# Optimization experiments

Measured on AMD Instinct MI355X. Metric: run time of the kernel, lower is better.

## Reference

```python
import jax, jax.numpy as jnp
import numpy as np
from jax import lax

WIN = 7            # skimage default win_size
K1, K2 = 0.01, 0.03
DATA_RANGE = 1.0


def _uniform_filter_valid(x):
    # (skimage uses reflect-padded uniform_filter then crops pad=3, which equals
    #  a valid windowed mean.)
    c, h, w = x.shape
    x4 = x[:, None]                                   # (C,1,H,W)
    kh = jnp.full((1, 1, WIN, 1), 1.0 / WIN, x.dtype)
    kw = jnp.full((1, 1, 1, WIN), 1.0 / WIN, x.dtype)
    dn = ('NCHW', 'OIHW', 'NCHW')
    x4 = lax.conv_general_dilated(x4, kh, (1, 1), 'VALID', dimension_numbers=dn)
    x4 = lax.conv_general_dilated(x4, kw, (1, 1), 'VALID', dimension_numbers=dn)
    return x4[:, 0]


def setup_inputs() -> dict:
    key = jax.random.key(0)
    k1, k2 = jax.random.split(key)
    shape = (32, 3, 512, 512)
    return {
        'input_tensor': jax.random.uniform(k1, shape, dtype=jnp.float32),
        'target': jax.random.uniform(k2, shape, dtype=jnp.float32),
    }


def reference(input_tensor, target):
    h, w = input_tensor.shape[-2:]
    x = input_tensor.reshape(-1, h, w).astype(jnp.float32)
    y = target.reshape(-1, h, w).astype(jnp.float32)

    C1 = (K1 * DATA_RANGE) ** 2
    C2 = (K2 * DATA_RANGE) ** 2
    NP = WIN * WIN
    cov_norm = NP / (NP - 1.0)  # sample covariance (skimage default)

    ux = _uniform_filter_valid(x)
    uy = _uniform_filter_valid(y)
    uxx = _uniform_filter_valid(x * x)
    uyy = _uniform_filter_valid(y * y)
    uxy = _uniform_filter_valid(x * y)

    vx = cov_norm * (uxx - ux * ux)
    vy = cov_norm * (uyy - uy * uy)
    vxy = cov_norm * (uxy - ux * uy)

    S = ((2.0 * ux * uy + C1) * (2.0 * vxy + C2)) / (
        (ux * ux + uy * uy + C1) * (vx + vy + C2))
    # mean over cropped spatial map per channel, then over channels == global mean
    return jnp.mean(S)
```

## Files before the change

### kernel.cpp

```cpp
#include <hip/hip_runtime.h>


namespace {
constexpr int W      = 512;
constexpr int HH     = 512;
constexpr int NIMG   = 96;
constexpr int OW     = 506;
constexpr int RSTRIP = 23;
constexpr int NSTRIP = 22;
constexpr float D1      = 0.2401f;
constexpr float D2      = 2.1609f;
constexpr float COVN    = 49.0f / 48.0f;
constexpr float COV2    = 2.0f * COVN;
constexpr float K49COV  = 49.0f * COVN;
constexpr float K49COV2 = 2.0f * 49.0f * COVN;
constexpr double NPIX   = 96.0 * 506.0 * 506.0;
}

__global__ __launch_bounds__(64, 3) void ssim_main(const float* __restrict__ X,
                                                   const float* __restrict__ Y,
                                                   double* __restrict__ acc)
{
    const int lane = threadIdx.x;
    const int img  = blockIdx.y;
    const int r0   = blockIdx.x * RSTRIP;
    const int c0   = lane * 8;

    const float* xb = X + (size_t)img * (W * HH) + c0;
    const float* yb = Y + (size_t)img * (W * HH) + c0;

    float V[5][8];
#pragma unroll
    for (int q = 0; q < 5; q++)
#pragma unroll
        for (int i = 0; i < 8; i++) V[q][i] = 0.0f;

    float xr[8], yr[8], xo[8], yo[8];

    auto load_row = [&](int r, float (&dx)[8], float (&dy)[8]) {
        const float* px = xb + (size_t)r * W;
        const float* py = yb + (size_t)r * W;
        float4 a = *(const float4*)px;
        float4 b = *(const float4*)(px + 4);
        dx[0] = a.x; dx[1] = a.y; dx[2] = a.z; dx[3] = a.w;
        dx[4] = b.x; dx[5] = b.y; dx[6] = b.z; dx[7] = b.w;
        float4 e = *(const float4*)py;
        float4 f = *(const float4*)(py + 4);
        dy[0] = e.x; dy[1] = e.y; dy[2] = e.z; dy[3] = e.w;
        dy[4] = f.x; dy[5] = f.y; dy[6] = f.z; dy[7] = f.w;
    };

#pragma unroll
    for (int k = 0; k < 6; k++) {
        load_row(r0 + k, xr, yr);
#pragma unroll
        for (int i = 0; i < 8; i++) {
            V[0][i] += xr[i];
            V[1][i] += yr[i];
            V[2][i] = fmaf(xr[i], xr[i], V[2][i]);
            V[3][i] = fmaf(yr[i], yr[i], V[3][i]);
            V[4][i] = fmaf(xr[i], yr[i], V[4][i]);
        }
    }
    load_row(r0 + 6, xr, yr);

    float sacc = 0.0f;

    for (int j = 0; j < RSTRIP; j++) {
#pragma unroll
        for (int i = 0; i < 8; i++) {
            V[0][i] += xr[i];
            V[1][i] += yr[i];
            V[2][i] = fmaf(xr[i], xr[i], V[2][i]);
            V[3][i] = fmaf(yr[i], yr[i], V[3][i]);
            V[4][i] = fmaf(xr[i], yr[i], V[4][i]);
        }

        load_row(r0 + j, xo, yo);
        int rn = r0 + j + 7; if (rn > HH - 1) rn = HH - 1;
        load_row(rn, xr, yr);

        float Vh[5][6];
#pragma unroll
        for (int q = 0; q < 5; q++)
#pragma unroll
            for (int i = 0; i < 6; i++) Vh[q][i] = __shfl_down(V[q][i], 1);

        float H[5];
#pragma unroll
        for (int q = 0; q < 5; q++)
            H[q] = ((V[q][0] + V[q][1]) + (V[q][2] + V[q][3])) +
                   ((V[q][4] + V[q][5]) + V[q][6]);

#pragma unroll
        for (int i = 0; i < 8; i++) {
            float U0 = H[0], U1 = H[1], U2 = H[2], U3 = H[3], U4 = H[4];
            float A    = U0 * U1;
            float q01  = fmaf(U0, U0, U1 * U1);
            float num1 = fmaf(2.0f, A, D1);
            float den1 = q01 + D1;
            float num2 = fmaf(K49COV2, U4, fmaf(-COV2, A, D2));
            float s23  = U2 + U3;
            float den2 = fmaf(K49COV, s23, fmaf(-COVN, q01, D2));
            float S = (num1 * num2) * __builtin_amdgcn_rcpf(den1 * den2);
            sacc += (c0 + i < OW) ? S : 0.0f;
            if (i < 7) {
#pragma unroll
                for (int q = 0; q < 5; q++) {
                    float addv = (i == 0) ? V[q][7] : Vh[q][i - 1];
                    H[q] += addv - V[q][i];
                }
            }
        }

#pragma unroll
        for (int i = 0; i < 8; i++) {
            V[0][i] -= xo[i];
            V[1][i] -= yo[i];
            V[2][i] = fmaf(-xo[i], xo[i], V[2][i]);
            V[3][i] = fmaf(-yo[i], yo[i], V[3][i]);
            V[4][i] = fmaf(-xo[i], yo[i], V[4][i]);
        }
    }

#pragma unroll
    for (int off = 32; off > 0; off >>= 1)
        sacc += __shfl_down(sacc, off);
    if (lane == 0) atomicAdd(acc, (double)sacc);
}

__global__ void ssim_finalize(const double* __restrict__ acc, float* __restrict__ out)
{
    out[0] = (float)(acc[0] / NPIX);
}

extern "C" void kernel_launch(void* const* d_in, const int* in_sizes, int n_in,
                              void* d_out, int out_size, void* d_ws, size_t ws_size,
                              hipStream_t stream)
{
    const float* X = (const float*)d_in[0];
    const float* Y = (const float*)d_in[1];
    float* out = (float*)d_out;
    double* acc = (double*)d_ws;

    hipMemsetAsync(d_ws, 0, sizeof(double), stream);
    ssim_main<<<dim3(NSTRIP, NIMG), 64, 0, stream>>>(X, Y, acc);
    ssim_finalize<<<1, 1, 0, stream>>>(acc, out);
}
```

Measured before the change: 253.1 us.

## Process two output rows per iteration with two-row-ahead prefetch and full unroll

Restructures the sliding-window loop to handle two output rows per iteration, loading two old and two new rows at a time so more memory loads are in flight ahead of use. The strip is re-split to 22 rows across 23 strips so the row count is even, and the loop is fully unrolled. Occupancy hint is relaxed from 3 to 2 waves per SIMD to allow more registers for the larger prefetch buffers. This trades occupancy and code size for deeper per-thread memory-level parallelism.

```diff
diff --git a/kernel.cpp b/kernel.cpp
--- a/kernel.cpp
+++ b/kernel.cpp
@@ -6,8 +6,8 @@
 constexpr int HH     = 512;
 constexpr int NIMG   = 96;
 constexpr int OW     = 506;
-constexpr int RSTRIP = 23;
-constexpr int NSTRIP = 22;
+constexpr int RSTRIP = 22;
+constexpr int NSTRIP = 23;
 constexpr float D1      = 0.2401f;
 constexpr float D2      = 2.1609f;
 constexpr float COVN    = 49.0f / 48.0f;
@@ -17,7 +17,7 @@
 constexpr double NPIX   = 96.0 * 506.0 * 506.0;
 }
 
-__global__ __launch_bounds__(64, 3) void ssim_main(const float* __restrict__ X,
+__global__ __launch_bounds__(64, 2) void ssim_main(const float* __restrict__ X,
                                                    const float* __restrict__ Y,
                                                    double* __restrict__ acc)
 {
@@ -35,63 +35,61 @@
 #pragma unroll
         for (int i = 0; i < 8; i++) V[q][i] = 0.0f;
 
-    float xr[8], yr[8], xo[8], yo[8];
-
-    auto load_row = [&](int r, float (&dx)[8], float (&dy)[8]) {
-        const float* px = xb + (size_t)r * W;
-        const float* py = yb + (size_t)r * W;
-        float4 a = *(const float4*)px;
-        float4 b = *(const float4*)(px + 4);
-        dx[0] = a.x; dx[1] = a.y; dx[2] = a.z; dx[3] = a.w;
-        dx[4] = b.x; dx[5] = b.y; dx[6] = b.z; dx[7] = b.w;
-        float4 e = *(const float4*)py;
-        float4 f = *(const float4*)(py + 4);
-        dy[0] = e.x; dy[1] = e.y; dy[2] = e.z; dy[3] = e.w;
-        dy[4] = f.x; dy[5] = f.y; dy[6] = f.z; dy[7] = f.w;
+    auto load2 = [&](int r, float (&dx)[2][8], float (&dy)[2][8]) {
+        int ra = r;     if (ra > HH - 1) ra = HH - 1;
+        int rb = r + 1; if (rb > HH - 1) rb = HH - 1;
+        const float* pxa = xb + (size_t)ra * W;
+        const float* pxb = xb + (size_t)rb * W;
+        const float* pya = yb + (size_t)ra * W;
+        const float* pyb = yb + (size_t)rb * W;
+        float4 a0 = *(const float4*)pxa, a1 = *(const float4*)(pxa + 4);
+        float4 b0 = *(const float4*)pxb, b1 = *(const float4*)(pxb + 4);
+        float4 e0 = *(const float4*)pya, e1 = *(const float4*)(pya + 4);
+        float4 f0 = *(const float4*)pyb, f1 = *(const float4*)(pyb + 4);
+        dx[0][0]=a0.x; dx[0][1]=a0.y; dx[0][2]=a0.z; dx[0][3]=a0.w;
+        dx[0][4]=a1.x; dx[0][5]=a1.y; dx[0][6]=a1.z; dx[0][7]=a1.w;
+        dx[1][0]=b0.x; dx[1][1]=b0.y; dx[1][2]=b0.z; dx[1][3]=b0.w;
+        dx[1][4]=b1.x; dx[1][5]=b1.y; dx[1][6]=b1.z; dx[1][7]=b1.w;
+        dy[0][0]=e0.x; dy[0][1]=e0.y; dy[0][2]=e0.z; dy[0][3]=e0.w;
+        dy[0][4]=e1.x; dy[0][5]=e1.y; dy[0][6]=e1.z; dy[0][7]=e1.w;
+        dy[1][0]=f0.x; dy[1][1]=f0.y; dy[1][2]=f0.z; dy[1][3]=f0.w;
+        dy[1][4]=f1.x; dy[1][5]=f1.y; dy[1][6]=f1.z; dy[1][7]=f1.w;
     };
 
-#pragma unroll
-    for (int k = 0; k < 6; k++) {
-        load_row(r0 + k, xr, yr);
+    auto vadd = [&](const float (&xs)[8], const float (&ys)[8]) {
 #pragma unroll
         for (int i = 0; i < 8; i++) {
-            V[0][i] += xr[i];
-            V[1][i] += yr[i];
-            V[2][i] = fmaf(xr[i], xr[i], V[2][i]);
-            V[3][i] = fmaf(yr[i], yr[i], V[3][i]);
-            V[4][i] = fmaf(xr[i], yr[i], V[4][i]);
+            V[0][i] += xs[i];
+            V[1][i] += ys[i];
+            V[2][i] = fmaf(xs[i], xs[i], V[2][i]);
+            V[3][i] = fmaf(ys[i], ys[i], V[3][i]);
+            V[4][i] = fmaf(xs[i], ys[i], V[4][i]);
         }
-    }
-    load_row(r0 + 6, xr, yr);
+    };
+    auto vsub = [&](const float (&xs)[8], const float (&ys)[8]) {
+#pragma unroll
+        for (int i = 0; i < 8; i++) {
+            V[0][i] -= xs[i];
+            V[1][i] -= ys[i];
+            V[2][i] = fmaf(-xs[i], xs[i], V[2][i]);
+            V[3][i] = fmaf(-ys[i], ys[i], V[3][i]);
+            V[4][i] = fmaf(-xs[i], ys[i], V[4][i]);
+        }
+    };
 
     float sacc = 0.0f;
 
-    for (int j = 0; j < RSTRIP; j++) {
-#pragma unroll
-        for (int i = 0; i < 8; i++) {
-            V[0][i] += xr[i];
-            V[1][i] += yr[i];
-            V[2][i] = fmaf(xr[i], xr[i], V[2][i]);
-            V[3][i] = fmaf(yr[i], yr[i], V[3][i]);
-            V[4][i] = fmaf(xr[i], yr[i], V[4][i]);
-        }
-
-        load_row(r0 + j, xo, yo);
-        int rn = r0 + j + 7; if (rn > HH - 1) rn = HH - 1;
-        load_row(rn, xr, yr);
-
+    auto ssim_row = [&]() {
         float Vh[5][6];
 #pragma unroll
         for (int q = 0; q < 5; q++)
 #pragma unroll
             for (int i = 0; i < 6; i++) Vh[q][i] = __shfl_down(V[q][i], 1);
-
         float H[5];
 #pragma unroll
         for (int q = 0; q < 5; q++)
             H[q] = ((V[q][0] + V[q][1]) + (V[q][2] + V[q][3])) +
                    ((V[q][4] + V[q][5]) + V[q][6]);
-
 #pragma unroll
         for (int i = 0; i < 8; i++) {
             float U0 = H[0], U1 = H[1], U2 = H[2], U3 = H[3], U4 = H[4];
@@ -112,14 +110,40 @@
                 }
             }
         }
+    };
+
+    {
+        float tx[2][8], ty[2][8];
+#pragma unroll
+        for (int k = 0; k < 3; k++) {
+            load2(r0 + 2 * k, tx, ty);
+            vadd(tx[0], ty[0]);
+            vadd(tx[1], ty[1]);
+        }
+    }
+
+    float xc[2][8], yc[2][8];
+    load2(r0 + 6, xc, yc);
+
+#pragma unroll
+    for (int jj = 0; jj < RSTRIP / 2; jj++) {
+        const int j0 = r0 + 2 * jj;
+
+        float xo[2][8], yo[2][8], xn[2][8], yn[2][8];
+        load2(j0, xo, yo);
+        load2(j0 + 8, xn, yn);
+
+        vadd(xc[0], yc[0]);
+        ssim_row();
+        vadd(xc[1], yc[1]);
+        vsub(xo[0], yo[0]);
+        ssim_row();
+        vsub(xo[1], yo[1]);
 
 #pragma unroll
         for (int i = 0; i < 8; i++) {
-            V[0][i] -= xo[i];
-            V[1][i] -= yo[i];
-            V[2][i] = fmaf(-xo[i], xo[i], V[2][i]);
-            V[3][i] = fmaf(-yo[i], yo[i], V[3][i]);
-            V[4][i] = fmaf(-xo[i], yo[i], V[4][i]);
+            xc[0][i] = xn[0][i]; xc[1][i] = xn[1][i];
+            yc[0][i] = yn[0][i]; yc[1][i] = yn[1][i];
         }
     }
 
```

Measured after the change: 251.8 us. About the same (-0.5%).

## Cache sliding-window rows in LDS ring buffer and lengthen row strips

Applied to the files above, without the earlier changes.

Rows that leave the vertical 7-row window are now read back from a per-block shared-memory ring buffer instead of being fetched again from global memory, which roughly halves global loads per output row. Strips are doubled to 46 rows, halving the grid and the redundant 6-row warmup per strip, and accumulation is spread over per-image atomics to reduce contention on one address. In exchange the grid has fewer blocks (11x96) and each block uses 32KB of LDS, which may limit occupancy and latency hiding.

```diff
diff --git a/kernel.cpp b/kernel.cpp
--- a/kernel.cpp
+++ b/kernel.cpp
@@ -6,8 +6,8 @@
 constexpr int HH     = 512;
 constexpr int NIMG   = 96;
 constexpr int OW     = 506;
-constexpr int RSTRIP = 23;
-constexpr int NSTRIP = 22;
+constexpr int RSTRIP = 46;
+constexpr int NSTRIP = 11;
 constexpr float D1      = 0.2401f;
 constexpr float D2      = 2.1609f;
 constexpr float COVN    = 49.0f / 48.0f;
@@ -17,10 +17,12 @@
 constexpr double NPIX   = 96.0 * 506.0 * 506.0;
 }
 
-__global__ __launch_bounds__(64, 3) void ssim_main(const float* __restrict__ X,
-                                                   const float* __restrict__ Y,
-                                                   double* __restrict__ acc)
+__global__ __launch_bounds__(64) void ssim_main(const float* __restrict__ X,
+                                                const float* __restrict__ Y,
+                                                double* __restrict__ acc)
 {
+    __shared__ float ring[8 * 1024];
+
     const int lane = threadIdx.x;
     const int img  = blockIdx.y;
     const int r0   = blockIdx.x * RSTRIP;
@@ -29,15 +31,18 @@
     const float* xb = X + (size_t)img * (W * HH) + c0;
     const float* yb = Y + (size_t)img * (W * HH) + c0;
 
+    float* ringx = &ring[c0];
+    float* ringy = &ring[512 + c0];
+
     float V[5][8];
 #pragma unroll
     for (int q = 0; q < 5; q++)
 #pragma unroll
         for (int i = 0; i < 8; i++) V[q][i] = 0.0f;
 
-    float xr[8], yr[8], xo[8], yo[8];
+    float xr[8], yr[8];
 
-    auto load_row = [&](int r, float (&dx)[8], float (&dy)[8]) {
+    auto gload_row = [&](int r, float (&dx)[8], float (&dy)[8]) {
         const float* px = xb + (size_t)r * W;
         const float* py = yb + (size_t)r * W;
         float4 a = *(const float4*)px;
@@ -49,36 +54,58 @@
         dy[0] = e.x; dy[1] = e.y; dy[2] = e.z; dy[3] = e.w;
         dy[4] = f.x; dy[5] = f.y; dy[6] = f.z; dy[7] = f.w;
     };
+    auto ring_write = [&](int slot, const float (&dx)[8], const float (&dy)[8]) {
+        float* px = ringx + slot * 1024;
+        float* py = ringy + slot * 1024;
+        *(float4*)(px)     = make_float4(dx[0], dx[1], dx[2], dx[3]);
+        *(float4*)(px + 4) = make_float4(dx[4], dx[5], dx[6], dx[7]);
+        *(float4*)(py)     = make_float4(dy[0], dy[1], dy[2], dy[3]);
+        *(float4*)(py + 4) = make_float4(dy[4], dy[5], dy[6], dy[7]);
+    };
+    auto ring_read = [&](int slot, float (&dx)[8], float (&dy)[8]) {
+        const float* px = ringx + slot * 1024;
+        const float* py = ringy + slot * 1024;
+        float4 a = *(const float4*)px;
+        float4 b = *(const float4*)(px + 4);
+        dx[0] = a.x; dx[1] = a.y; dx[2] = a.z; dx[3] = a.w;
+        dx[4] = b.x; dx[5] = b.y; dx[6] = b.z; dx[7] = b.w;
+        float4 e = *(const float4*)py;
+        float4 f = *(const float4*)(py + 4);
+        dy[0] = e.x; dy[1] = e.y; dy[2] = e.z; dy[3] = e.w;
+        dy[4] = f.x; dy[5] = f.y; dy[6] = f.z; dy[7] = f.w;
+    };
+    auto vadd = [&](const float (&xs)[8], const float (&ys)[8]) {
+#pragma unroll
+        for (int i = 0; i < 8; i++) {
+            V[0][i] += xs[i];
+            V[1][i] += ys[i];
+            V[2][i] = fmaf(xs[i], xs[i], V[2][i]);
+            V[3][i] = fmaf(ys[i], ys[i], V[3][i]);
+            V[4][i] = fmaf(xs[i], ys[i], V[4][i]);
+        }
+    };
 
 #pragma unroll
     for (int k = 0; k < 6; k++) {
-        load_row(r0 + k, xr, yr);
-#pragma unroll
-        for (int i = 0; i < 8; i++) {
-            V[0][i] += xr[i];
-            V[1][i] += yr[i];
-            V[2][i] = fmaf(xr[i], xr[i], V[2][i]);
-            V[3][i] = fmaf(yr[i], yr[i], V[3][i]);
-            V[4][i] = fmaf(xr[i], yr[i], V[4][i]);
-        }
+        gload_row(r0 + k, xr, yr);
+        vadd(xr, yr);
+        ring_write(k, xr, yr);
     }
-    load_row(r0 + 6, xr, yr);
+    gload_row(r0 + 6, xr, yr);
 
     float sacc = 0.0f;
 
+#pragma unroll 2
     for (int j = 0; j < RSTRIP; j++) {
-#pragma unroll
-        for (int i = 0; i < 8; i++) {
-            V[0][i] += xr[i];
-            V[1][i] += yr[i];
-            V[2][i] = fmaf(xr[i], xr[i], V[2][i]);
-            V[3][i] = fmaf(yr[i], yr[i], V[3][i]);
-            V[4][i] = fmaf(xr[i], yr[i], V[4][i]);
-        }
+        vadd(xr, yr);
+        ring_write((j + 6) & 7, xr, yr);
 
-        load_row(r0 + j, xo, yo);
         int rn = r0 + j + 7; if (rn > HH - 1) rn = HH - 1;
-        load_row(rn, xr, yr);
+        float xn[8], yn[8];
+        gload_row(rn, xn, yn);
+
+        float xo[8], yo[8];
+        ring_read(j & 7, xo, yo);
 
         float Vh[5][6];
 #pragma unroll
@@ -121,17 +148,22 @@
             V[3][i] = fmaf(-yo[i], yo[i], V[3][i]);
             V[4][i] = fmaf(-xo[i], yo[i], V[4][i]);
         }
+
+#pragma unroll
+        for (int i = 0; i < 8; i++) { xr[i] = xn[i]; yr[i] = yn[i]; }
     }
 
 #pragma unroll
     for (int off = 32; off > 0; off >>= 1)
         sacc += __shfl_down(sacc, off);
-    if (lane == 0) atomicAdd(acc, (double)sacc);
+    if (lane == 0) atomicAdd(&acc[img], (double)sacc);
 }
 
 __global__ void ssim_finalize(const double* __restrict__ acc, float* __restrict__ out)
 {
-    out[0] = (float)(acc[0] / NPIX);
+    double s = 0.0;
+    for (int i = 0; i < NIMG; i++) s += acc[i];
+    out[0] = (float)(s / NPIX);
 }
 
 extern "C" void kernel_launch(void* const* d_in, const int* in_sizes, int n_in,
@@ -143,7 +175,7 @@
     float* out = (float*)d_out;
     double* acc = (double*)d_ws;
 
-    hipMemsetAsync(d_ws, 0, sizeof(double), stream);
+    hipMemsetAsync(d_ws, 0, NIMG * sizeof(double), stream);
     ssim_main<<<dim3(NSTRIP, NIMG), 64, 0, stream>>>(X, Y, acc);
     ssim_finalize<<<1, 1, 0, stream>>>(acc, out);
 }
```

Measured after the change: 258.4 us. 1.02x slower.
